# Kernel optimization log

Hardware: AMD Instinct MI355X
Metric: run time of the kernel (lower is better)

The kernel has to match this reference:

```python
import jax, jax.numpy as jnp
import numpy as np
import math

_OFFSETS = sorted(set(range(0, 33)) | {48, 64, 96, 128, 192, 256, 384, 512, 768, 1024, 1536})
B, N, D, H, FFN = 1, 2048, 1024, 16, 2816
EPS = 1e-6


def _rmsnorm(x, scale):
    rms = jnp.sqrt(jnp.mean(x * x, axis=-1, keepdims=True) + EPS)
    return scale * (x / rms)


def setup_inputs() -> dict:
    key = jax.random.key(0)
    ks = jax.random.split(key, 8)
    s = 0.02
    alphas = jnp.linspace(0.2, 2.0, H)
    delta_vals = jnp.array([math.log(1.0 + max(d, 0.2)) for d in _OFFSETS], dtype=jnp.float32)
    pos_bias = -delta_vals[:, None] * alphas[None, :]  # (n_offsets, H)
    return {
        "x": jax.random.normal(ks[0], (B, N, D), jnp.float32),
        "norm1_scale": jnp.ones((D,), jnp.float32),
        "norm2_scale": jnp.ones((D,), jnp.float32),
        "w_qkv": jax.random.normal(ks[1], (D, 3 * D), jnp.float32) * s,
        "w_out": jax.random.normal(ks[2], (D, D), jnp.float32) * s,
        "w_gate": jax.random.normal(ks[3], (D, D), jnp.float32) * s,
        "b_gate": jnp.full((D,), 2.0, jnp.float32),
        "pos_bias": pos_bias,
        "w_ffn_gate": jax.random.normal(ks[4], (D, FFN), jnp.float32) * s,
        "w_ffn_up": jax.random.normal(ks[5], (D, FFN), jnp.float32) * s,
        "w_ffn_down": jax.random.normal(ks[6], (FFN, D), jnp.float32) * s,
        "offsets": jnp.array(_OFFSETS, dtype=jnp.int32),
    }


def reference(x, norm1_scale, norm2_scale, w_qkv, w_out, w_gate, b_gate,
              pos_bias, w_ffn_gate, w_ffn_up, w_ffn_down, offsets):
    Bx, Nx, Dx = x.shape
    HD = Dx // H
    # --- attention branch: x + attn(norm1(x)) ---
    xn = _rmsnorm(x, norm1_scale)
    qkv = xn @ w_qkv
    q, k, v = jnp.split(qkv, 3, axis=-1)
    to_heads = lambda t: t.reshape(Bx, Nx, H, HD).transpose(0, 2, 1, 3)  # (B,H,N,HD)
    q, k, v = to_heads(q), to_heads(k), to_heads(v)

    t_idx = jnp.arange(Nx)
    # gather positions t-delta per (query t, offset o); clamped positions are masked below
    src = jnp.clip(t_idx[:, None] - offsets[None, :], 0, None)  # (N, O)
    Kg = k[:, :, src, :]  # (B,H,N,O,HD)
    Vg = v[:, :, src, :]

    scale = HD ** (-0.5)
    scores = jnp.einsum('bhnd,bhnod->bhno', q, Kg) * scale
    scores = scores + pos_bias.T[None, :, None, :]  # (1,H,1,O)
    invalid = t_idx[:, None] < offsets[None, :]      # (N, O)
    scores = jnp.where(invalid[None, None], -jnp.inf, scores)
    alpha = jax.nn.softmax(scores, axis=-1)
    out = jnp.einsum('bhno,bhnod->bhnd', alpha, Vg)
    out = out.transpose(0, 2, 1, 3).reshape(Bx, Nx, Dx)

    gate = jax.nn.sigmoid(xn @ w_gate + b_gate)
    x = x + (out * gate) @ w_out

    # --- FFN branch: x + SwiGLU(norm2(x)) ---
    xn2 = _rmsnorm(x, norm2_scale)
    x = x + (jax.nn.silu(xn2 @ w_ffn_gate) * (xn2 @ w_ffn_up)) @ w_ffn_down
    return x
```

## Files before the change

kernel.cpp:

```cpp
#include <hip/hip_runtime.h>
#include <hip/hip_bf16.h>
#include <math.h>

typedef __bf16 bf16;
typedef __bf16 v8bf __attribute__((ext_vector_type(8)));
typedef __bf16 v4bf __attribute__((ext_vector_type(4)));
typedef float v4f __attribute__((ext_vector_type(4)));

#define N_TOK 2048
#define DIM 1024
#define NH 16
#define FFN_DIM 2816

#define GLL(g, l) __builtin_amdgcn_global_load_lds(                         \
    (const __attribute__((address_space(1))) uint32_t*)(g),                 \
    (__attribute__((address_space(3))) uint32_t*)(l), 16, 0, 0)

__global__ __launch_bounds__(256) void transpose_all_kernel(
    const float* __restrict__ w_qkv, const float* __restrict__ w_gate,
    const float* __restrict__ w_out, const float* __restrict__ w_ffng,
    const float* __restrict__ w_ffnu, const float* __restrict__ w_ffnd,
    bf16* __restrict__ wqkvgT, bf16* __restrict__ woutT,
    bf16* __restrict__ wcatT, bf16* __restrict__ wffndT)
{
    int bid = blockIdx.x;
    const float* W; bf16* D; int Kd, Nc, nb, kb, dstbase;
    if (bid < 3072) {
        W = w_qkv; D = wqkvgT; Kd = 1024; Nc = 3072;
        nb = (bid % 96) * 32; kb = (bid / 96) * 32; dstbase = nb;
    } else if (bid < 4096) { int b = bid - 3072;
        W = w_gate; D = wqkvgT; Kd = 1024; Nc = 1024;
        nb = (b % 32) * 32; kb = (b / 32) * 32; dstbase = 3072 + nb;
    } else if (bid < 5120) { int b = bid - 4096;
        W = w_out; D = woutT; Kd = 1024; Nc = 1024;
        nb = (b % 32) * 32; kb = (b / 32) * 32; dstbase = nb;
    } else if (bid < 7936) { int b = bid - 5120;
        W = w_ffng; D = wcatT; Kd = 1024; Nc = 2816;
        nb = (b % 88) * 32; kb = (b / 88) * 32;
        dstbase = (nb >> 6) * 128 + (nb & 63);
    } else if (bid < 10752) { int b = bid - 7936;
        W = w_ffnu; D = wcatT; Kd = 1024; Nc = 2816;
        nb = (b % 88) * 32; kb = (b / 88) * 32;
        dstbase = (nb >> 6) * 128 + 64 + (nb & 63);
    } else { int b = bid - 10752;
        W = w_ffnd; D = wffndT; Kd = 2816; Nc = 1024;
        nb = (b % 32) * 32; kb = (b / 32) * 32; dstbase = nb;
    }
    __shared__ float tile[32][33];
    int tx = threadIdx.x, ty = threadIdx.y;
#pragma unroll
    for (int r = 0; r < 4; ++r)
        tile[ty + r * 8][tx] = W[(size_t)(kb + ty + r * 8) * Nc + nb + tx];
    __syncthreads();
#pragma unroll
    for (int r = 0; r < 4; ++r)
        D[(size_t)(dstbase + ty + r * 8) * Kd + kb + tx] = (bf16)tile[tx][ty + r * 8];
}

__global__ __launch_bounds__(256) void rmsnorm_kernel(
    const float* __restrict__ x, const float* __restrict__ scale, bf16* __restrict__ out)
{
    int row = blockIdx.x, tid = threadIdx.x;
    float4 v = ((const float4*)(x + (size_t)row * DIM))[tid];
    float ss = v.x * v.x + v.y * v.y + v.z * v.z + v.w * v.w;
#pragma unroll
    for (int off = 32; off > 0; off >>= 1) ss += __shfl_down(ss, off);
    __shared__ float ps[4];
    if ((tid & 63) == 0) ps[tid >> 6] = ss;
    __syncthreads();
    float tot = ps[0] + ps[1] + ps[2] + ps[3];
    float inv = rsqrtf(tot * (1.0f / DIM) + 1e-6f);
    float4 s = ((const float4*)scale)[tid];
    union { bf16 b[4]; uint2 u; } p;
    p.b[0] = (bf16)(v.x * inv * s.x);
    p.b[1] = (bf16)(v.y * inv * s.y);
    p.b[2] = (bf16)(v.z * inv * s.z);
    p.b[3] = (bf16)(v.w * inv * s.w);
    ((uint2*)(out + (size_t)row * DIM))[tid] = p.u;
}

__global__ __launch_bounds__(256) void attn_kernel(
    const bf16* __restrict__ qkvg, const int* __restrict__ offs,
    const float* __restrict__ pos_bias, bf16* __restrict__ attgb)
{
    constexpr int O = 44;
    const int t = blockIdx.x, tid = threadIdx.x;
    const int wv = tid >> 6, lane = tid & 63;
    const int h1 = lane >> 2, l4 = lane & 3;
    const size_t RS = 4 * DIM;
    __shared__ float sS[O][17];
    __shared__ float sPB[O * 16];
    __shared__ int so[O];
    if (tid < O) so[tid] = offs[tid];
    for (int i = tid; i < O * 16; i += 256) sPB[i] = pos_bias[i];
    __syncthreads();

    const bf16* qbase = qkvg + (size_t)t * RS + h1 * 64;
    v8bf q0v = *(const v8bf*)(qbase + l4 * 8);
    v8bf q1v = *(const v8bf*)(qbase + 32 + l4 * 8);
    float qa[16];
#pragma unroll
    for (int e = 0; e < 8; ++e) {
        qa[e] = (float)q0v[e] * 0.125f;
        qa[8 + e] = (float)q1v[e] * 0.125f;
    }

#pragma unroll 4
    for (int it = 0; it < 11; ++it) {
        const int o = it * 4 + wv;
        const int src = t - so[o];
        const int srcc = src < 0 ? 0 : src;
        const bf16* kbase = qkvg + (size_t)srcc * RS + DIM + h1 * 64;
        v8bf k0 = *(const v8bf*)(kbase + l4 * 8);
        v8bf k1 = *(const v8bf*)(kbase + 32 + l4 * 8);
        float p = 0.f;
#pragma unroll
        for (int e = 0; e < 8; ++e)
            p += qa[e] * (float)k0[e];
#pragma unroll
        for (int e = 0; e < 8; ++e)
            p += qa[8 + e] * (float)k1[e];
        p += __shfl_xor(p, 1);
        p += __shfl_xor(p, 2);
        float s = (src >= 0) ? p + sPB[o * NH + h1] : -INFINITY;
        if (l4 == 0) sS[o][h1] = s;
    }
    __syncthreads();

    const int h = tid >> 4, j16 = tid & 15;
    float mx = -INFINITY;
#pragma unroll
    for (int o = j16; o < O; o += 16) mx = fmaxf(mx, sS[o][h]);
    mx = fmaxf(mx, __shfl_xor(mx, 1));
    mx = fmaxf(mx, __shfl_xor(mx, 2));
    mx = fmaxf(mx, __shfl_xor(mx, 4));
    mx = fmaxf(mx, __shfl_xor(mx, 8));
    float sum = 0.f;
#pragma unroll
    for (int o = j16; o < O; o += 16) {
        float e = __expf(sS[o][h] - mx);
        sS[o][h] = e;
        sum += e;
    }
    sum += __shfl_xor(sum, 1);
    sum += __shfl_xor(sum, 2);
    sum += __shfl_xor(sum, 4);
    sum += __shfl_xor(sum, 8);
    float inv = 1.0f / sum;
    __syncthreads();

    float a0 = 0.f, a1 = 0.f, a2 = 0.f, a3 = 0.f;
#pragma unroll 4
    for (int o = 0; o < O; ++o) {
        int src = t - so[o];
        int srcc = src < 0 ? 0 : src;
        float a = sS[o][h];
        v4bf vv = *(const v4bf*)(qkvg + (size_t)srcc * RS + 2 * DIM + tid * 4);
        a0 += a * (float)vv[0];
        a1 += a * (float)vv[1];
        a2 += a * (float)vv[2];
        a3 += a * (float)vv[3];
    }
    v4bf gv = *(const v4bf*)(qkvg + (size_t)t * RS + 3 * DIM + tid * 4);
    v4bf ov;
    ov[0] = (bf16)(a0 * inv * (float)gv[0]);
    ov[1] = (bf16)(a1 * inv * (float)gv[1]);
    ov[2] = (bf16)(a2 * inv * (float)gv[2]);
    ov[3] = (bf16)(a3 * inv * (float)gv[3]);
    *(v4bf*)(attgb + (size_t)t * DIM + tid * 4) = ov;
}

template<int BM, int BN, int NTHR, int EPI>
__global__ __launch_bounds__(NTHR) void gemm_kernel(
    const bf16* __restrict__ A, const bf16* __restrict__ Bt,
    int M, int N, int K,
    float* __restrict__ outf, bf16* __restrict__ outb,
    const float* __restrict__ e1, const float* __restrict__ bias)
{
    constexpr int WAVES = NTHR / 64;
    constexpr int WCOLS = WAVES / 2;
    constexpr int WME = BM / 2;
    constexpr int WNE = BN / WCOLS;
    constexpr int MI = WME / 16;
    constexpr int NJ = WNE / 16;
    constexpr int STAGE_BYTES = 2 * (BM + BN) * 32 * 2;
    constexpr int EPI_BYTES = (EPI == 6) ? BM * 66 * 4 : 0;
    constexpr int SMEM_BYTES = STAGE_BYTES > EPI_BYTES ? STAGE_BYTES : EPI_BYTES;
    __shared__ __align__(16) char smem[SMEM_BYTES];
    bf16* AsB = (bf16*)smem;
    bf16* BsB = (bf16*)(smem + 2 * BM * 32 * 2);

    const int tid = threadIdx.x;
    const int m0 = blockIdx.y * BM, n0 = blockIdx.x * BN;
    const int lane = tid & 63, wave = tid >> 6;
    const int wr = wave / WCOLS, wc = wave % WCOLS;
    const int wm = wr * WME, wn = wc * WNE;
    const int lrow = lane & 15, l16 = lane >> 4;

    const int srow = tid >> 2;
    const int gcol = ((tid & 3) ^ ((srow >> 1) & 3)) * 8;
    const int lofs = srow * 32 + (tid & 3) * 8;
    const bf16* gA = A + (size_t)(m0 + srow) * K + gcol;
    const bf16* gB = Bt + (size_t)(n0 + srow) * K + gcol;

    auto STAGE = [&](int b, int kt) {
        const int ko = kt * 32;
        GLL(gA + ko, AsB + b * BM * 32 + lofs);
        GLL(gB + ko, BsB + b * BN * 32 + lofs);
    };

    v4f acc[MI][NJ] = {};
    auto COMPUTE = [&](int b) {
        v8bf af[MI], bfr[NJ];
#pragma unroll
        for (int i = 0; i < MI; ++i) {
            int r = wm + i * 16 + lrow;
            af[i] = *(v8bf*)&AsB[b * BM * 32 + r * 32 + ((l16 ^ ((r >> 1) & 3)) * 8)];
        }
#pragma unroll
        for (int j = 0; j < NJ; ++j) {
            int r = wn + j * 16 + lrow;
            bfr[j] = *(v8bf*)&BsB[b * BN * 32 + r * 32 + ((l16 ^ ((r >> 1) & 3)) * 8)];
        }
        __builtin_amdgcn_s_setprio(1);
#pragma unroll
        for (int i = 0; i < MI; ++i)
#pragma unroll
            for (int j = 0; j < NJ; ++j)
                acc[i][j] = __builtin_amdgcn_mfma_f32_16x16x32_bf16(af[i], bfr[j], acc[i][j], 0, 0, 0);
        __builtin_amdgcn_s_setprio(0);
    };

    const int NT = K >> 5;
    STAGE(0, 0); STAGE(1, 1);
    for (int t = 0; t < NT; ++t) {
        if (t < NT - 1) asm volatile("s_waitcnt vmcnt(2)" ::: "memory");
        else            asm volatile("s_waitcnt vmcnt(0)" ::: "memory");
        __builtin_amdgcn_s_barrier();
        __builtin_amdgcn_sched_barrier(0);
        COMPUTE(t & 1);
        __builtin_amdgcn_sched_barrier(0);
        __builtin_amdgcn_s_barrier();
        if (t + 2 < NT) STAGE(t & 1, t + 2);
    }

    if constexpr (EPI == 6) {
        float* eps = (float*)smem;
        const bool isGate = (wn < 64);
        if (isGate) {
#pragma unroll
            for (int i = 0; i < MI; ++i)
#pragma unroll
                for (int j = 0; j < NJ; ++j)
#pragma unroll
                    for (int r = 0; r < 4; ++r) {
                        int rowL = wm + i * 16 + l16 * 4 + r;
                        int colL = wn + j * 16 + lrow;
                        eps[rowL * 66 + colL] = acc[i][j][r];
                    }
        }
        __builtin_amdgcn_s_barrier();
        if (!isGate) {
            const int halfN = N >> 1;
#pragma unroll
            for (int i = 0; i < MI; ++i)
#pragma unroll
                for (int j = 0; j < NJ; ++j)
#pragma unroll
                    for (int r = 0; r < 4; ++r) {
                        int rowL = wm + i * 16 + l16 * 4 + r;
                        int colU = wn - 64 + j * 16 + lrow;
                        float g = eps[rowL * 66 + colU];
                        float sil = g / (1.0f + __expf(-g));
                        float u = acc[i][j][r];
                        outb[(size_t)(m0 + rowL) * halfN + (n0 >> 1) + colU] = (bf16)(sil * u);
                    }
        }
        return;
    }

#pragma unroll
    for (int i = 0; i < MI; ++i)
#pragma unroll
        for (int j = 0; j < NJ; ++j)
#pragma unroll
            for (int r = 0; r < 4; ++r) {
                int row = m0 + wm + i * 16 + l16 * 4 + r;
                int col = n0 + wn + j * 16 + lrow;
                size_t idx = (size_t)row * N + col;
                float v = acc[i][j][r];
                if constexpr (EPI == 3) {
                    outf[idx] = e1[idx] + v;
                } else if constexpr (EPI == 5) {
                    if (col >= 3 * DIM) {
                        float g = 1.0f / (1.0f + __expf(-(v + bias[col - 3 * DIM])));
                        outb[idx] = (bf16)g;
                    } else {
                        outb[idx] = (bf16)v;
                    }
                }
            }
}

extern "C" void kernel_launch(void* const* d_in, const int* in_sizes, int n_in,
                              void* d_out, int out_size, void* d_ws, size_t ws_size,
                              hipStream_t stream)
{
    const float* x        = (const float*)d_in[0];
    const float* n1s      = (const float*)d_in[1];
    const float* n2s      = (const float*)d_in[2];
    const float* w_qkv    = (const float*)d_in[3];
    const float* w_out    = (const float*)d_in[4];
    const float* w_gate   = (const float*)d_in[5];
    const float* b_gate   = (const float*)d_in[6];
    const float* pos_bias = (const float*)d_in[7];
    const float* w_ffng   = (const float*)d_in[8];
    const float* w_ffnu   = (const float*)d_in[9];
    const float* w_ffnd   = (const float*)d_in[10];
    const int* offsets    = (const int*)d_in[11];
    float* out = (float*)d_out;

    char* ws = (char*)d_ws;
    size_t cur = 0;
    auto alloc = [&](size_t bytes) -> void* {
        void* p = ws + cur;
        cur += (bytes + 255) & ~(size_t)255;
        return p;
    };
    bf16*  xnb    = (bf16*)alloc((size_t)N_TOK * DIM * 2);
    bf16*  qkvgb  = (bf16*)alloc((size_t)N_TOK * 4 * DIM * 2);
    bf16*  attgb  = (bf16*)alloc((size_t)N_TOK * DIM * 2);
    float* x1     = (float*)alloc((size_t)N_TOK * DIM * 4);
    bf16*  xn2b   = (bf16*)alloc((size_t)N_TOK * DIM * 2);
    bf16*  hb     = (bf16*)alloc((size_t)N_TOK * FFN_DIM * 2);
    bf16*  wqkvgT = (bf16*)alloc((size_t)4 * DIM * DIM * 2);
    bf16*  woutT  = (bf16*)alloc((size_t)DIM * DIM * 2);
    bf16*  wcatT  = (bf16*)alloc((size_t)2 * FFN_DIM * DIM * 2);
    bf16*  wffndT = (bf16*)alloc((size_t)FFN_DIM * DIM * 2);

    transpose_all_kernel<<<13568, dim3(32, 8), 0, stream>>>(
        w_qkv, w_gate, w_out, w_ffng, w_ffnu, w_ffnd,
        wqkvgT, woutT, wcatT, wffndT);

    rmsnorm_kernel<<<N_TOK, 256, 0, stream>>>(x, n1s, xnb);
    gemm_kernel<128, 128, 512, 5><<<dim3(32, 16), 512, 0, stream>>>(
        xnb, wqkvgT, N_TOK, 4 * DIM, DIM, nullptr, qkvgb, nullptr, b_gate);
    attn_kernel<<<dim3(N_TOK), 256, 0, stream>>>(qkvgb, offsets, pos_bias, attgb);
    gemm_kernel<64, 64, 256, 3><<<dim3(16, 32), 256, 0, stream>>>(
        attgb, woutT, N_TOK, DIM, DIM, x1, nullptr, x, nullptr);
    rmsnorm_kernel<<<N_TOK, 256, 0, stream>>>(x1, n2s, xn2b);
    gemm_kernel<128, 128, 512, 6><<<dim3(44, 16), 512, 0, stream>>>(
        xn2b, wcatT, N_TOK, 2 * FFN_DIM, DIM, nullptr, hb, nullptr, nullptr);
    gemm_kernel<64, 64, 256, 3><<<dim3(16, 32), 256, 0, stream>>>(
        hb, wffndT, N_TOK, DIM, FFN_DIM, out, nullptr, x1, nullptr);
}
```

Baseline: 151.0 us.

## Add multi-buffer GEMM pipeline, retile GEMMs, and split attention V-accumulation across waves

```diff
diff --git a/kernel.cpp b/kernel.cpp
--- a/kernel.cpp
+++ b/kernel.cpp
@@ -15,6 +15,18 @@
 #define GLL(g, l) __builtin_amdgcn_global_load_lds(                         \
     (const __attribute__((address_space(1))) uint32_t*)(g),                 \
     (__attribute__((address_space(3))) uint32_t*)(l), 16, 0, 0)
+
+#define WAITV(n) do {                                                        \
+    switch (n) {                                                             \
+    case 0: asm volatile("s_waitcnt vmcnt(0)" ::: "memory"); break;          \
+    case 2: asm volatile("s_waitcnt vmcnt(2)" ::: "memory"); break;          \
+    case 3: asm volatile("s_waitcnt vmcnt(3)" ::: "memory"); break;          \
+    case 4: asm volatile("s_waitcnt vmcnt(4)" ::: "memory"); break;          \
+    case 6: asm volatile("s_waitcnt vmcnt(6)" ::: "memory"); break;          \
+    case 8: asm volatile("s_waitcnt vmcnt(8)" ::: "memory"); break;          \
+    case 9: asm volatile("s_waitcnt vmcnt(9)" ::: "memory"); break;          \
+    default: asm volatile("s_waitcnt vmcnt(0)" ::: "memory"); break; }       \
+} while (0)
 
 __global__ __launch_bounds__(256) void transpose_all_kernel(
     const float* __restrict__ w_qkv, const float* __restrict__ w_gate,
@@ -91,6 +103,7 @@
     __shared__ float sS[O][17];
     __shared__ float sPB[O * 16];
     __shared__ int so[O];
+    __shared__ float sAcc[4 * 1024];
     if (tid < O) so[tid] = offs[tid];
     for (int i = tid; i < O * 16; i += 256) sPB[i] = pos_bias[i];
     __syncthreads();
@@ -115,11 +128,9 @@
         v8bf k1 = *(const v8bf*)(kbase + 32 + l4 * 8);
         float p = 0.f;
 #pragma unroll
-        for (int e = 0; e < 8; ++e)
-            p += qa[e] * (float)k0[e];
-#pragma unroll
-        for (int e = 0; e < 8; ++e)
-            p += qa[8 + e] * (float)k1[e];
+        for (int e = 0; e < 8; ++e) p += qa[e] * (float)k0[e];
+#pragma unroll
+        for (int e = 0; e < 8; ++e) p += qa[8 + e] * (float)k1[e];
         p += __shfl_xor(p, 1);
         p += __shfl_xor(p, 2);
         float s = (src >= 0) ? p + sPB[o * NH + h1] : -INFINITY;
@@ -149,28 +160,48 @@
     float inv = 1.0f / sum;
     __syncthreads();
 
-    float a0 = 0.f, a1 = 0.f, a2 = 0.f, a3 = 0.f;
+    const int h2 = lane >> 2;
+    const int dbase = lane * 16;
+    float pacc[16] = {};
 #pragma unroll 4
-    for (int o = 0; o < O; ++o) {
+    for (int it = 0; it < 11; ++it) {
+        int o = it * 4 + wv;
         int src = t - so[o];
         int srcc = src < 0 ? 0 : src;
-        float a = sS[o][h];
-        v4bf vv = *(const v4bf*)(qkvg + (size_t)srcc * RS + 2 * DIM + tid * 4);
-        a0 += a * (float)vv[0];
-        a1 += a * (float)vv[1];
-        a2 += a * (float)vv[2];
-        a3 += a * (float)vv[3];
-    }
+        float a = sS[o][h2];
+        const bf16* vb = qkvg + (size_t)srcc * RS + 2 * DIM + dbase;
+        v8bf v0 = *(const v8bf*)(vb);
+        v8bf v1 = *(const v8bf*)(vb + 8);
+#pragma unroll
+        for (int e = 0; e < 8; ++e) {
+            pacc[e] += a * (float)v0[e];
+            pacc[8 + e] += a * (float)v1[e];
+        }
+    }
+#pragma unroll
+    for (int q = 0; q < 4; ++q) {
+        int phys = lane * 4 + (q ^ (lane & 3));
+        *(float4*)&sAcc[wv * 1024 + phys * 4] =
+            make_float4(pacc[q * 4], pacc[q * 4 + 1], pacc[q * 4 + 2], pacc[q * 4 + 3]);
+    }
+    __syncthreads();
+
+    const int lr = tid >> 2, qr = tid & 3;
+    const int phys = lr * 4 + (qr ^ (lr & 3));
+    float4 p0 = *(const float4*)&sAcc[0 * 1024 + phys * 4];
+    float4 p1 = *(const float4*)&sAcc[1 * 1024 + phys * 4];
+    float4 p2 = *(const float4*)&sAcc[2 * 1024 + phys * 4];
+    float4 p3 = *(const float4*)&sAcc[3 * 1024 + phys * 4];
     v4bf gv = *(const v4bf*)(qkvg + (size_t)t * RS + 3 * DIM + tid * 4);
     v4bf ov;
-    ov[0] = (bf16)(a0 * inv * (float)gv[0]);
-    ov[1] = (bf16)(a1 * inv * (float)gv[1]);
-    ov[2] = (bf16)(a2 * inv * (float)gv[2]);
-    ov[3] = (bf16)(a3 * inv * (float)gv[3]);
+    ov[0] = (bf16)((p0.x + p1.x + p2.x + p3.x) * inv * (float)gv[0]);
+    ov[1] = (bf16)((p0.y + p1.y + p2.y + p3.y) * inv * (float)gv[1]);
+    ov[2] = (bf16)((p0.z + p1.z + p2.z + p3.z) * inv * (float)gv[2]);
+    ov[3] = (bf16)((p0.w + p1.w + p2.w + p3.w) * inv * (float)gv[3]);
     *(v4bf*)(attgb + (size_t)t * DIM + tid * 4) = ov;
 }
 
-template<int BM, int BN, int NTHR, int EPI>
+template<int BM, int BN, int NTHR, int NBUF, int EPI>
 __global__ __launch_bounds__(NTHR) void gemm_kernel(
     const bf16* __restrict__ A, const bf16* __restrict__ Bt,
     int M, int N, int K,
@@ -183,12 +214,14 @@
     constexpr int WNE = BN / WCOLS;
     constexpr int MI = WME / 16;
     constexpr int NJ = WNE / 16;
-    constexpr int STAGE_BYTES = 2 * (BM + BN) * 32 * 2;
+    constexpr int CH_A = BM * 4, CH_B = BN * 4;
+    constexpr int LPT = (CH_A + CH_B) / NTHR;
+    constexpr int STAGE_BYTES = NBUF * (BM + BN) * 32 * 2;
     constexpr int EPI_BYTES = (EPI == 6) ? BM * 66 * 4 : 0;
     constexpr int SMEM_BYTES = STAGE_BYTES > EPI_BYTES ? STAGE_BYTES : EPI_BYTES;
     __shared__ __align__(16) char smem[SMEM_BYTES];
     bf16* AsB = (bf16*)smem;
-    bf16* BsB = (bf16*)(smem + 2 * BM * 32 * 2);
+    bf16* BsB = (bf16*)(smem + NBUF * BM * 32 * 2);
 
     const int tid = threadIdx.x;
     const int m0 = blockIdx.y * BM, n0 = blockIdx.x * BN;
@@ -197,16 +230,29 @@
     const int wm = wr * WME, wn = wc * WNE;
     const int lrow = lane & 15, l16 = lane >> 4;
 
-    const int srow = tid >> 2;
-    const int gcol = ((tid & 3) ^ ((srow >> 1) & 3)) * 8;
-    const int lofs = srow * 32 + (tid & 3) * 8;
-    const bf16* gA = A + (size_t)(m0 + srow) * K + gcol;
-    const bf16* gB = Bt + (size_t)(n0 + srow) * K + gcol;
+    const bf16* gptr[LPT];
+    int lo[LPT];
+    bool pa[LPT];
+#pragma unroll
+    for (int i = 0; i < LPT; ++i) {
+        int c = tid + i * NTHR;
+        bool inA = c < CH_A;
+        int cc = inA ? c : c - CH_A;
+        int r = cc >> 2, q = cc & 3;
+        int gq = (q ^ ((r >> 1) & 3)) * 8;
+        gptr[i] = inA ? A + (size_t)(m0 + r) * K + gq
+                      : Bt + (size_t)(n0 + r) * K + gq;
+        lo[i] = r * 32 + q * 8;
+        pa[i] = inA;
+    }
 
     auto STAGE = [&](int b, int kt) {
         const int ko = kt * 32;
-        GLL(gA + ko, AsB + b * BM * 32 + lofs);
-        GLL(gB + ko, BsB + b * BN * 32 + lofs);
+#pragma unroll
+        for (int i = 0; i < LPT; ++i) {
+            bf16* dst = (pa[i] ? AsB + b * BM * 32 : BsB + b * BN * 32) + lo[i];
+            GLL(gptr[i] + ko, dst);
+        }
     };
 
     v4f acc[MI][NJ] = {};
@@ -232,16 +278,26 @@
     };
 
     const int NT = K >> 5;
-    STAGE(0, 0); STAGE(1, 1);
-    for (int t = 0; t < NT; ++t) {
-        if (t < NT - 1) asm volatile("s_waitcnt vmcnt(2)" ::: "memory");
-        else            asm volatile("s_waitcnt vmcnt(0)" ::: "memory");
+#pragma unroll
+    for (int i = 0; i < NBUF; ++i) STAGE(i, i);
+    for (int t = 0; t < NT - (NBUF - 1); ++t) {
+        WAITV((NBUF - 1) * LPT);
         __builtin_amdgcn_s_barrier();
         __builtin_amdgcn_sched_barrier(0);
-        COMPUTE(t & 1);
+        COMPUTE(t & (NBUF - 1));
         __builtin_amdgcn_sched_barrier(0);
         __builtin_amdgcn_s_barrier();
-        if (t + 2 < NT) STAGE(t & 1, t + 2);
+        if (t + NBUF < NT) STAGE(t & (NBUF - 1), t + NBUF);
+    }
+#pragma unroll
+    for (int e = NBUF - 1; e >= 1; --e) {
+        const int t = NT - e;
+        WAITV((e - 1) * LPT);
+        __builtin_amdgcn_s_barrier();
+        __builtin_amdgcn_sched_barrier(0);
+        COMPUTE(t & (NBUF - 1));
+        __builtin_amdgcn_sched_barrier(0);
+        __builtin_amdgcn_s_barrier();
     }
 
     if constexpr (EPI == 6) {
@@ -259,6 +315,7 @@
                         eps[rowL * 66 + colL] = acc[i][j][r];
                     }
         }
+        asm volatile("s_waitcnt lgkmcnt(0)" ::: "memory");
         __builtin_amdgcn_s_barrier();
         if (!isGate) {
             const int halfN = N >> 1;
@@ -343,14 +400,14 @@
         wqkvgT, woutT, wcatT, wffndT);
 
     rmsnorm_kernel<<<N_TOK, 256, 0, stream>>>(x, n1s, xnb);
-    gemm_kernel<128, 128, 512, 5><<<dim3(32, 16), 512, 0, stream>>>(
+    gemm_kernel<64, 128, 256, 2, 5><<<dim3(32, 32), 256, 0, stream>>>(
         xnb, wqkvgT, N_TOK, 4 * DIM, DIM, nullptr, qkvgb, nullptr, b_gate);
     attn_kernel<<<dim3(N_TOK), 256, 0, stream>>>(qkvgb, offsets, pos_bias, attgb);
-    gemm_kernel<64, 64, 256, 3><<<dim3(16, 32), 256, 0, stream>>>(
+    gemm_kernel<64, 64, 256, 4, 3><<<dim3(16, 32), 256, 0, stream>>>(
         attgb, woutT, N_TOK, DIM, DIM, x1, nullptr, x, nullptr);
     rmsnorm_kernel<<<N_TOK, 256, 0, stream>>>(x1, n2s, xn2b);
-    gemm_kernel<128, 128, 512, 6><<<dim3(44, 16), 512, 0, stream>>>(
+    gemm_kernel<64, 128, 256, 2, 6><<<dim3(44, 32), 256, 0, stream>>>(
         xn2b, wcatT, N_TOK, 2 * FFN_DIM, DIM, nullptr, hb, nullptr, nullptr);
-    gemm_kernel<64, 64, 256, 3><<<dim3(16, 32), 256, 0, stream>>>(
+    gemm_kernel<64, 64, 256, 4, 3><<<dim3(16, 32), 256, 0, stream>>>(
         hb, wffndT, N_TOK, DIM, FFN_DIM, out, nullptr, x1, nullptr);
 }
```

Result: slower. 167.0 us (+10.7%).
